# Kernel optimization log

Hardware: AMD Instinct MI355X
Metric: run time of the kernel (lower is better)

The kernel has to match this reference:

```python
import jax, jax.numpy as jnp
import numpy as np

TIMESTEPS = 1000

def _cosine_schedule(T, s=0.008):
    # Nichol & Dhariwal cosine schedule
    x = np.linspace(0.0, T, T + 1, dtype=np.float64)
    acp = np.cos(((x / T) + s) / (1.0 + s) * np.pi / 2.0) ** 2
    acp = acp / acp[0]
    betas = np.clip(1.0 - acp[1:] / acp[:-1], 1e-4, 0.999)
    alphas_cumprod = np.cumprod(1.0 - betas)
    return (betas.astype(np.float32),
            np.sqrt(alphas_cumprod).astype(np.float32),
            np.sqrt(1.0 - alphas_cumprod).astype(np.float32))

BETAS, SQRT_ACP, SQRT_OM_ACP = _cosine_schedule(TIMESTEPS)

B = 2048            # crystals
N_PER = 64          # atoms per crystal (uniform ragged groups)
N = B * N_PER       # total atoms
NODE_DIM = 64
N_SPECIES = 100

def setup_inputs() -> dict:
    key = jax.random.key(0)
    ks = jax.random.split(key, 10)
    frac_coords = jax.random.uniform(ks[0], (N, 3), dtype=jnp.float32)
    noise = jax.random.normal(ks[1], (N, 3), dtype=jnp.float32)
    pred_noise = jax.random.normal(ks[2], (N, 3), dtype=jnp.float32)
    h_final = jax.random.normal(ks[3], (N, NODE_DIM), dtype=jnp.float32)
    # lattice: identity-dominated cells ~5 Angstrom with small perturbation
    lattice = 5.0 * jnp.eye(3, dtype=jnp.float32)[None] + 0.2 * jax.random.normal(ks[4], (B, 3, 3), dtype=jnp.float32)
    W1 = jax.random.normal(ks[5], (NODE_DIM, 128), dtype=jnp.float32) * (1.0 / np.sqrt(NODE_DIM))
    b1 = jnp.zeros((128,), dtype=jnp.float32)
    W2 = jax.random.normal(ks[6], (128, N_SPECIES), dtype=jnp.float32) * (1.0 / np.sqrt(128.0))
    b2 = jnp.zeros((N_SPECIES,), dtype=jnp.float32)
    t = jax.random.randint(ks[7], (B,), 0, TIMESTEPS)
    batch_indices = jnp.repeat(jnp.arange(B), N_PER)
    species = jax.random.randint(ks[8], (N,), 0, N_SPECIES)
    return {"frac_coords": frac_coords, "noise": noise, "pred_noise": pred_noise,
            "h_final": h_final, "lattice": lattice, "W1": W1, "b1": b1,
            "W2": W2, "b2": b2, "t": t, "batch_indices": batch_indices,
            "species": species}

def reference(frac_coords, noise, pred_noise, h_final, lattice, W1, b1, W2, b2,
              t, batch_indices, species):
    sqrt_acp = jnp.asarray(SQRT_ACP)
    sqrt_om = jnp.asarray(SQRT_OM_ACP)
    t_nodes = t[batch_indices]                       # [N]
    sa = sqrt_acp[t_nodes][:, None]                  # [N,1]
    so = sqrt_om[t_nodes][:, None]                   # [N,1]
    # q_sample + periodic wrap
    x_t = sa * frac_coords + so * noise
    x_t = x_t - jnp.floor(x_t)
    # diffusion MSE (dynamics output pred_noise supplied as input)
    loss_diffusion = jnp.mean((pred_noise - noise) ** 2)
    # predicted x0, wrapped
    pred_x0 = (x_t - so * pred_noise) / sa
    pred_x0 = pred_x0 - jnp.floor(pred_x0)
    # vectorized ragged PBC repulsion (uniform groups of N_PER atoms)
    bsz = lattice.shape[0]
    n = frac_coords.shape[0] // bsz
    f = pred_x0.reshape(bsz, n, 3)                   # [B,n,3]
    diff = f[:, :, None, :] - f[:, None, :, :]       # [B,n,n,3]
    diff = diff - jnp.round(diff)                    # minimum-image convention
    diff_c = jnp.einsum('bijk,bkl->bijl', diff, lattice)
    dist_sq = jnp.sum(diff_c ** 2, axis=-1)          # [B,n,n]
    eye = jnp.eye(n, dtype=bool)
    dist_sq = jnp.where(eye[None], 1e10, dist_sq)    # fill_diagonal_(inf)
    dist = jnp.sqrt(dist_sq + 1e-8)
    rep = jax.nn.relu(0.8 - dist) ** 2
    l_repulsion = jnp.sum(rep) / n / bsz
    loss_diffusion = loss_diffusion + 5.0 * l_repulsion
    # species head: Linear -> SiLU -> Linear, cross entropy
    hidden = jax.nn.silu(h_final @ W1 + b1)
    logits = hidden @ W2 + b2                        # [N,100]
    logp = jax.nn.log_softmax(logits, axis=-1)
    loss_species = -jnp.mean(jnp.take_along_axis(logp, species[:, None], axis=-1))
    return (loss_diffusion, loss_species, l_repulsion)
```

## Files before the change

kernel.cpp:

```cpp
#include <hip/hip_runtime.h>
#include <math.h>

#define TSTEPS   1000
#define NB       2048
#define NPER     64
#define NATOMS   (NB*NPER)
#define NDIM     64
#define NHID     128
#define NSPEC    100
#define H_LD     136
#define H_LDS_SHORTS (64*H_LD)

typedef __attribute__((ext_vector_type(8))) short bf16x8;
typedef __attribute__((ext_vector_type(4))) float f32x4;

__device__ inline short f2bf(float x) {
  unsigned u = __builtin_bit_cast(unsigned, x);
  u += 0x7fffu + ((u >> 16) & 1u);
  return (short)(u >> 16);
}

__global__ __launch_bounds__(256) void k_sched(float* __restrict__ sacp,
                                               float* __restrict__ som,
                                               const float* __restrict__ W1,
                                               const float* __restrict__ W2,
                                               unsigned short* __restrict__ w1f,
                                               unsigned short* __restrict__ w2f) {
  const int tid = threadIdx.x, blk = blockIdx.x;
  if (blk == 0) {
    __shared__ double sh[256];
    const double PI = 3.14159265358979323846, s = 0.008;
    const int t0 = tid * 4;
    double lg[4], loc = 0.0;
    if (t0 < TSTEPS) {
      double c[5];
      #pragma unroll
      for (int i = 0; i < 5; ++i) {
        double u = (((double)(t0 + i) / (double)TSTEPS) + s) / (1.0 + s) * PI * 0.5;
        c[i] = cos(u);
      }
      #pragma unroll
      for (int i = 0; i < 4; ++i) {
        double beta = 1.0 - (c[i+1]*c[i+1]) / (c[i]*c[i]);
        beta = fmin(fmax(beta, 1e-4), 0.999);
        lg[i] = log(1.0 - beta);
        loc += lg[i];
      }
    }
    sh[tid] = loc;
    __syncthreads();
    for (int off = 1; off < 256; off <<= 1) {
      double add = (tid >= off) ? sh[tid - off] : 0.0;
      __syncthreads();
      sh[tid] += add;
      __syncthreads();
    }
    if (t0 < TSTEPS) {
      double run = sh[tid] - loc;
      #pragma unroll
      for (int i = 0; i < 4; ++i) {
        run += lg[i];
        double cum = exp(run);
        sacp[t0+i] = (float)sqrt(cum);
        som[t0+i]  = (float)sqrt(1.0 - cum);
      }
    }
  } else if (blk <= 4) {
    const int c0 = (blk - 1) * 256 + tid;
    const int lane = c0 & 63, t = c0 >> 6;
    const int kk = t & 1, nt = t >> 1;
    const int q = lane >> 4, l15 = lane & 15;
    __attribute__((aligned(16))) unsigned short v[8];
    #pragma unroll
    for (int j = 0; j < 8; ++j) {
      int k = kk*32 + q*8 + j;
      v[j] = (unsigned short)f2bf(W1[k*NHID + nt*16 + l15]);
    }
    *(uint4*)(w1f + (size_t)c0*8) = *(const uint4*)v;
  } else {
    for (int c0 = (blk - 5) * 256 + tid; c0 < 3584; c0 += 1792) {
      const int lane = c0 & 63, t = c0 >> 6;
      const int kk = t & 3, nt = t >> 2;
      const int q = lane >> 4, l15 = lane & 15;
      const int cls = nt*16 + l15;
      __attribute__((aligned(16))) unsigned short v[8];
      #pragma unroll
      for (int j = 0; j < 8; ++j) {
        int k = kk*32 + q*8 + j;
        v[j] = (cls < NSPEC) ? (unsigned short)f2bf(W2[k*NSPEC + cls]) : 0;
      }
      *(uint4*)(w2f + (size_t)c0*8) = *(const uint4*)v;
    }
  }
}

__global__ __launch_bounds__(256, 4) void k_main(const float* __restrict__ hfin,
                                                 const float* __restrict__ b1,
                                                 const float* __restrict__ b2,
                                                 const int*   __restrict__ spec,
                                                 const unsigned short* __restrict__ w1f,
                                                 const unsigned short* __restrict__ w2f,
                                                 const float* __restrict__ frac,
                                                 const float* __restrict__ noise,
                                                 const float* __restrict__ pnoise,
                                                 const float* __restrict__ lattice,
                                                 const int*   __restrict__ tarr,
                                                 const float* __restrict__ sacp,
                                                 const float* __restrict__ som,
                                                 float* __restrict__ mseP,
                                                 float* __restrict__ repP,
                                                 float* __restrict__ specP) {
  __shared__ __attribute__((aligned(16))) unsigned short Hs[H_LDS_SHORTS];
  __shared__ float f[NPER*3];
  __shared__ float wred[12];
  const int tid  = threadIdx.x;
  const int wave = tid >> 6, lane = tid & 63;
  const int q = lane >> 4, l15 = lane & 15;
  const int b = blockIdx.x, atomBase = b*64, slabBase = atomBase + wave*16;

  const int tt = tarr[b];
  const float sa = sacp[tt], so = som[tt];
  float msep = 0.0f;
  if (tid < NPER*3) {
    const int gi = b*(NPER*3) + tid;
    float fr = frac[gi], nz = noise[gi], p = pnoise[gi];
    float xt = sa*fr + so*nz;  xt -= floorf(xt);
    float px = (xt - so*p)/sa; px -= floorf(px);
    f[tid] = px;
    float d = p - nz; msep = d*d;
  }

  bf16x8 aF[2];
  {
    const float* rp = hfin + (size_t)(slabBase + l15) * NDIM;
    #pragma unroll
    for (int kk = 0; kk < 2; ++kk) {
      const float4 p = *(const float4*)(rp + kk*32 + q*8);
      const float4 r = *(const float4*)(rp + kk*32 + q*8 + 4);
      bf16x8 a;
      a[0]=f2bf(p.x); a[1]=f2bf(p.y); a[2]=f2bf(p.z); a[3]=f2bf(p.w);
      a[4]=f2bf(r.x); a[5]=f2bf(r.y); a[6]=f2bf(r.z); a[7]=f2bf(r.w);
      aF[kk] = a;
    }
  }

  f32x4 acc1[8];
  #pragma unroll
  for (int nt = 0; nt < 8; ++nt) acc1[nt] = (f32x4){0.f,0.f,0.f,0.f};
  #pragma unroll
  for (int nt = 0; nt < 8; ++nt) {
    #pragma unroll
    for (int kk = 0; kk < 2; ++kk) {
      bf16x8 wa = *(const bf16x8*)(w1f + (size_t)(((nt*2 + kk)*64 + lane))*8);
      acc1[nt] = __builtin_amdgcn_mfma_f32_16x16x32_bf16(wa, aF[kk], acc1[nt], 0, 0, 0);
    }
  }
  #pragma unroll
  for (int nt = 0; nt < 8; ++nt) {
    const float4 bv = *(const float4*)(b1 + nt*16 + q*4);
    float s0, s1, s2, s3;
    { float x = acc1[nt][0] + bv.x; s0 = x / (1.0f + __expf(-x)); }
    { float x = acc1[nt][1] + bv.y; s1 = x / (1.0f + __expf(-x)); }
    { float x = acc1[nt][2] + bv.z; s2 = x / (1.0f + __expf(-x)); }
    { float x = acc1[nt][3] + bv.w; s3 = x / (1.0f + __expf(-x)); }
    uint2 pk;
    pk.x = ((unsigned)(unsigned short)f2bf(s0)) | (((unsigned)(unsigned short)f2bf(s1)) << 16);
    pk.y = ((unsigned)(unsigned short)f2bf(s2)) | (((unsigned)(unsigned short)f2bf(s3)) << 16);
    *(uint2*)(Hs + (wave*16 + l15)*H_LD + nt*16 + q*4) = pk;
  }
  __syncthreads();

  bf16x8 a2[4];
  #pragma unroll
  for (int kk = 0; kk < 4; ++kk)
    a2[kk] = *(const bf16x8*)(Hs + (wave*16 + l15)*H_LD + kk*32 + q*8);
  f32x4 acc2[7];
  #pragma unroll
  for (int nt = 0; nt < 7; ++nt) acc2[nt] = (f32x4){0.f,0.f,0.f,0.f};
  #pragma unroll
  for (int nt = 0; nt < 7; ++nt) {
    #pragma unroll
    for (int kk = 0; kk < 4; ++kk) {
      bf16x8 wb = *(const bf16x8*)(w2f + (size_t)(((nt*4 + kk)*64 + lane))*8);
      acc2[nt] = __builtin_amdgcn_mfma_f32_16x16x32_bf16(wb, a2[kk], acc2[nt], 0, 0, 0);
    }
  }

  const int tgt = spec[slabBase + l15];
  float mx = -1e30f;
  #pragma unroll
  for (int nt = 0; nt < 7; ++nt) {
    float4 bb = {0.f,0.f,0.f,0.f};
    if (nt < 6 || q == 0) bb = *(const float4*)(b2 + nt*16 + q*4);
    #pragma unroll
    for (int r = 0; r < 4; ++r) {
      const int cls = nt*16 + q*4 + r;
      float v = acc2[nt][r] + ((const float*)&bb)[r];
      v = (cls < NSPEC) ? v : -1e30f;
      acc2[nt][r] = v;
      mx = fmaxf(mx, v);
    }
  }
  mx = fmaxf(mx, __shfl_xor(mx, 16, 64));
  mx = fmaxf(mx, __shfl_xor(mx, 32, 64));
  float ssum = 0.0f, lt = 0.0f;
  #pragma unroll
  for (int nt = 0; nt < 7; ++nt) {
    #pragma unroll
    for (int r = 0; r < 4; ++r) {
      float v = acc2[nt][r];
      ssum += __expf(v - mx);
      lt   += (nt*16 + q*4 + r == tgt) ? v : 0.0f;
    }
  }
  ssum += __shfl_xor(ssum, 16, 64);  ssum += __shfl_xor(ssum, 32, 64);
  lt   += __shfl_xor(lt,   16, 64);  lt   += __shfl_xor(lt,   32, 64);
  float logp = lt - mx - __logf(ssum);
  #pragma unroll
  for (int d = 1; d < 16; d <<= 1) logp += __shfl_xor(logp, d, 64);

  const float* L = lattice + b*9;
  const float L00=L[0],L01=L[1],L02=L[2],
              L10=L[3],L11=L[4],L12=L[5],
              L20=L[6],L21=L[7],L22=L[8];
  float rep = 0.0f;
  #pragma unroll 4
  for (int it = 0; it < 16; ++it) {
    const int i = it*4 + wave;
    const int j = lane;
    if (i != j) {
      float dx = f[i*3+0] - f[j*3+0]; dx -= rintf(dx);
      float dy = f[i*3+1] - f[j*3+1]; dy -= rintf(dy);
      float dz = f[i*3+2] - f[j*3+2]; dz -= rintf(dz);
      float cx = dx*L00 + dy*L10 + dz*L20;
      float cy = dx*L01 + dy*L11 + dz*L21;
      float cz = dx*L02 + dy*L12 + dz*L22;
      float dist = sqrtf(cx*cx + cy*cy + cz*cz + 1e-8f);
      float r = 0.8f - dist;
      if (r > 0.0f) rep = fmaf(r, r, rep);
    }
  }
  #pragma unroll
  for (int o = 32; o > 0; o >>= 1) {
    rep  += __shfl_down(rep,  o, 64);
    msep += __shfl_down(msep, o, 64);
  }
  if (lane == 0) { wred[wave] = logp; wred[4+wave] = rep; wred[8+wave] = msep; }
  __syncthreads();
  if (tid == 0) {
    specP[b] = wred[0] + wred[1] + wred[2]  + wred[3];
    repP[b]  = wred[4] + wred[5] + wred[6]  + wred[7];
    mseP[b]  = wred[8] + wred[9] + wred[10] + wred[11];
  }
}

__global__ __launch_bounds__(1024) void k_fin(const float* __restrict__ mseP,
                                              const float* __restrict__ repP,
                                              const float* __restrict__ specP,
                                              float* __restrict__ out) {
  __shared__ double sh[48];
  const int tid = threadIdx.x;
  double m = 0.0, r = 0.0, s = 0.0;
  for (int i = tid; i < NB; i += 1024) {
    m += (double)mseP[i];
    r += (double)repP[i];
    s += (double)specP[i];
  }
  #pragma unroll
  for (int o = 32; o > 0; o >>= 1) {
    m += __shfl_down(m, o, 64);
    r += __shfl_down(r, o, 64);
    s += __shfl_down(s, o, 64);
  }
  const int w = tid >> 6, lane = tid & 63;
  if (lane == 0) { sh[w] = m; sh[16+w] = r; sh[32+w] = s; }
  __syncthreads();
  if (tid == 0) {
    double M=0, R=0, S=0;
    for (int i = 0; i < 16; ++i) { M += sh[i]; R += sh[16+i]; S += sh[32+i]; }
    double mse   = M / (double)(NATOMS*3);
    double lrep  = R / (double)NATOMS;
    double lspec = -S / (double)NATOMS;
    out[0] = (float)(mse + 5.0*lrep);
    out[1] = (float)lspec;
    out[2] = (float)lrep;
  }
}

extern "C" void kernel_launch(void* const* d_in, const int* in_sizes, int n_in,
                              void* d_out, int out_size, void* d_ws, size_t ws_size,
                              hipStream_t stream) {
  const float* frac    = (const float*)d_in[0];
  const float* noise   = (const float*)d_in[1];
  const float* pnoise  = (const float*)d_in[2];
  const float* hfin    = (const float*)d_in[3];
  const float* lattice = (const float*)d_in[4];
  const float* W1      = (const float*)d_in[5];
  const float* b1      = (const float*)d_in[6];
  const float* W2      = (const float*)d_in[7];
  const float* b2      = (const float*)d_in[8];
  const int*   tarr    = (const int*)d_in[9];
  const int*   spec    = (const int*)d_in[11];
  float* out = (float*)d_out;

  float*  sacp = (float*)d_ws;
  float*  som  = sacp + 1024;
  unsigned short* w1f = (unsigned short*)((char*)d_ws + 8192);
  unsigned short* w2f = (unsigned short*)((char*)d_ws + 24576);
  float* mseP  = (float*)((char*)d_ws + 53248);
  float* repP  = (float*)((char*)d_ws + 61440);
  float* specP = (float*)((char*)d_ws + 69632);

  k_sched<<<dim3(12), dim3(256),  0, stream>>>(sacp, som, W1, W2, w1f, w2f);
  k_main <<<dim3(NB), dim3(256),  0, stream>>>(hfin, b1, b2, spec, w1f, w2f,
                                               frac, noise, pnoise, lattice,
                                               tarr, sacp, som, mseP, repP, specP);
  k_fin  <<<dim3(1),  dim3(1024), 0, stream>>>(mseP, repP, specP, out);
}
```

Baseline: 137.1 us.

## Remove block barriers in main kernel using per-wave LDS and shuffles

The block-wide __syncthreads calls are removed. Each wave now keeps its own LDS slice for the hidden activations, laid out to match the MFMA fragments, and uses only a wave barrier. Fractional coordinates stay in registers, one atom per lane, and are broadcast with shuffles for the repulsion loop. Per-wave partial sums go straight to global memory and are reduced in the final kernel. The change also pads b2 in the setup kernel, uses fast reciprocal and sqrt intrinsics, fully unrolls the pair loop, and drops the 4-blocks-per-CU launch bound, so register use may rise and occupancy may change.

```diff
diff --git a/kernel.cpp b/kernel.cpp
--- a/kernel.cpp
+++ b/kernel.cpp
@@ -8,8 +8,6 @@
 #define NDIM     64
 #define NHID     128
 #define NSPEC    100
-#define H_LD     136
-#define H_LDS_SHORTS (64*H_LD)
 
 typedef __attribute__((ext_vector_type(8))) short bf16x8;
 typedef __attribute__((ext_vector_type(4))) float f32x4;
@@ -24,10 +22,13 @@
                                                float* __restrict__ som,
                                                const float* __restrict__ W1,
                                                const float* __restrict__ W2,
+                                               const float* __restrict__ b2,
                                                unsigned short* __restrict__ w1f,
-                                               unsigned short* __restrict__ w2f) {
+                                               unsigned short* __restrict__ w2f,
+                                               float* __restrict__ b2p) {
   const int tid = threadIdx.x, blk = blockIdx.x;
   if (blk == 0) {
+    if (tid < 112) b2p[tid] = (tid < NSPEC) ? b2[tid] : 0.0f;
     __shared__ double sh[256];
     const double PI = 3.14159265358979323846, s = 0.008;
     const int t0 = tid * 4;
@@ -94,40 +95,46 @@
   }
 }
 
-__global__ __launch_bounds__(256, 4) void k_main(const float* __restrict__ hfin,
-                                                 const float* __restrict__ b1,
-                                                 const float* __restrict__ b2,
-                                                 const int*   __restrict__ spec,
-                                                 const unsigned short* __restrict__ w1f,
-                                                 const unsigned short* __restrict__ w2f,
-                                                 const float* __restrict__ frac,
-                                                 const float* __restrict__ noise,
-                                                 const float* __restrict__ pnoise,
-                                                 const float* __restrict__ lattice,
-                                                 const int*   __restrict__ tarr,
-                                                 const float* __restrict__ sacp,
-                                                 const float* __restrict__ som,
-                                                 float* __restrict__ mseP,
-                                                 float* __restrict__ repP,
-                                                 float* __restrict__ specP) {
-  __shared__ __attribute__((aligned(16))) unsigned short Hs[H_LDS_SHORTS];
-  __shared__ float f[NPER*3];
-  __shared__ float wred[12];
+__global__ __launch_bounds__(256) void k_main(const float* __restrict__ hfin,
+                                              const float* __restrict__ b1,
+                                              const float* __restrict__ b2p,
+                                              const int*   __restrict__ spec,
+                                              const unsigned short* __restrict__ w1f,
+                                              const unsigned short* __restrict__ w2f,
+                                              const float* __restrict__ frac,
+                                              const float* __restrict__ noise,
+                                              const float* __restrict__ pnoise,
+                                              const float* __restrict__ lattice,
+                                              const int*   __restrict__ tarr,
+                                              const float* __restrict__ sacp,
+                                              const float* __restrict__ som,
+                                              float* __restrict__ mseP,
+                                              float* __restrict__ repP,
+                                              float* __restrict__ specP) {
+  __shared__ __attribute__((aligned(16))) unsigned short Hs[4*2048];
   const int tid  = threadIdx.x;
   const int wave = tid >> 6, lane = tid & 63;
   const int q = lane >> 4, l15 = lane & 15;
   const int b = blockIdx.x, atomBase = b*64, slabBase = atomBase + wave*16;
+  unsigned short* HsW = Hs + wave*2048;
 
   const int tt = tarr[b];
   const float sa = sacp[tt], so = som[tt];
-  float msep = 0.0f;
-  if (tid < NPER*3) {
-    const int gi = b*(NPER*3) + tid;
-    float fr = frac[gi], nz = noise[gi], p = pnoise[gi];
-    float xt = sa*fr + so*nz;  xt -= floorf(xt);
-    float px = (xt - so*p)/sa; px -= floorf(px);
-    f[tid] = px;
-    float d = p - nz; msep = d*d;
+  const float rsa = __builtin_amdgcn_rcpf(sa);
+  float px0, px1, px2, msep;
+  {
+    const int a = atomBase + lane;
+    const float3 fr = *(const float3*)(frac   + 3*(size_t)a);
+    const float3 nz = *(const float3*)(noise  + 3*(size_t)a);
+    const float3 pn = *(const float3*)(pnoise + 3*(size_t)a);
+    float xt0 = fmaf(so, nz.x, sa*fr.x); xt0 -= floorf(xt0);
+    float xt1 = fmaf(so, nz.y, sa*fr.y); xt1 -= floorf(xt1);
+    float xt2 = fmaf(so, nz.z, sa*fr.z); xt2 -= floorf(xt2);
+    px0 = (xt0 - so*pn.x)*rsa; px0 -= floorf(px0);
+    px1 = (xt1 - so*pn.y)*rsa; px1 -= floorf(px1);
+    px2 = (xt2 - so*pn.z)*rsa; px2 -= floorf(px2);
+    float d0 = pn.x - nz.x, d1 = pn.y - nz.y, d2 = pn.z - nz.z;
+    msep = fmaf(d0, d0, fmaf(d1, d1, d2*d2));
   }
 
   bf16x8 aF[2];
@@ -158,22 +165,24 @@
   #pragma unroll
   for (int nt = 0; nt < 8; ++nt) {
     const float4 bv = *(const float4*)(b1 + nt*16 + q*4);
-    float s0, s1, s2, s3;
-    { float x = acc1[nt][0] + bv.x; s0 = x / (1.0f + __expf(-x)); }
-    { float x = acc1[nt][1] + bv.y; s1 = x / (1.0f + __expf(-x)); }
-    { float x = acc1[nt][2] + bv.z; s2 = x / (1.0f + __expf(-x)); }
-    { float x = acc1[nt][3] + bv.w; s3 = x / (1.0f + __expf(-x)); }
+    float sl[4];
+    #pragma unroll
+    for (int r = 0; r < 4; ++r) {
+      float x = acc1[nt][r] + ((const float*)&bv)[r];
+      float e = __expf(-x);
+      sl[r] = x * __builtin_amdgcn_rcpf(1.0f + e);
+    }
     uint2 pk;
-    pk.x = ((unsigned)(unsigned short)f2bf(s0)) | (((unsigned)(unsigned short)f2bf(s1)) << 16);
-    pk.y = ((unsigned)(unsigned short)f2bf(s2)) | (((unsigned)(unsigned short)f2bf(s3)) << 16);
-    *(uint2*)(Hs + (wave*16 + l15)*H_LD + nt*16 + q*4) = pk;
-  }
-  __syncthreads();
+    pk.x = ((unsigned)(unsigned short)f2bf(sl[0])) | (((unsigned)(unsigned short)f2bf(sl[1])) << 16);
+    pk.y = ((unsigned)(unsigned short)f2bf(sl[2])) | (((unsigned)(unsigned short)f2bf(sl[3])) << 16);
+    *(uint2*)(HsW + (nt*2 + (q>>1))*128 + l15*8 + (q&1)*4) = pk;
+  }
+  __builtin_amdgcn_wave_barrier();
 
   bf16x8 a2[4];
   #pragma unroll
   for (int kk = 0; kk < 4; ++kk)
-    a2[kk] = *(const bf16x8*)(Hs + (wave*16 + l15)*H_LD + kk*32 + q*8);
+    a2[kk] = *(const bf16x8*)(HsW + (kk*4 + q)*128 + l15*8);
   f32x4 acc2[7];
   #pragma unroll
   for (int nt = 0; nt < 7; ++nt) acc2[nt] = (f32x4){0.f,0.f,0.f,0.f};
@@ -190,8 +199,7 @@
   float mx = -1e30f;
   #pragma unroll
   for (int nt = 0; nt < 7; ++nt) {
-    float4 bb = {0.f,0.f,0.f,0.f};
-    if (nt < 6 || q == 0) bb = *(const float4*)(b2 + nt*16 + q*4);
+    const float4 bb = *(const float4*)(b2p + nt*16 + q*4);
     #pragma unroll
     for (int r = 0; r < 4; ++r) {
       const int cls = nt*16 + q*4 + r;
@@ -224,19 +232,21 @@
               L10=L[3],L11=L[4],L12=L[5],
               L20=L[6],L21=L[7],L22=L[8];
   float rep = 0.0f;
-  #pragma unroll 4
+  #pragma unroll
   for (int it = 0; it < 16; ++it) {
-    const int i = it*4 + wave;
-    const int j = lane;
-    if (i != j) {
-      float dx = f[i*3+0] - f[j*3+0]; dx -= rintf(dx);
-      float dy = f[i*3+1] - f[j*3+1]; dy -= rintf(dy);
-      float dz = f[i*3+2] - f[j*3+2]; dz -= rintf(dz);
+    const int i = wave*16 + it;
+    float xi = __shfl(px0, i, 64);
+    float yi = __shfl(px1, i, 64);
+    float zi = __shfl(px2, i, 64);
+    if (i != lane) {
+      float dx = xi - px0; dx -= rintf(dx);
+      float dy = yi - px1; dy -= rintf(dy);
+      float dz = zi - px2; dz -= rintf(dz);
       float cx = dx*L00 + dy*L10 + dz*L20;
       float cy = dx*L01 + dy*L11 + dz*L21;
       float cz = dx*L02 + dy*L12 + dz*L22;
-      float dist = sqrtf(cx*cx + cy*cy + cz*cz + 1e-8f);
-      float r = 0.8f - dist;
+      float d2 = fmaf(cx, cx, fmaf(cy, cy, cz*cz)) + 1e-8f;
+      float r  = 0.8f - __builtin_amdgcn_sqrtf(d2);
       if (r > 0.0f) rep = fmaf(r, r, rep);
     }
   }
@@ -245,12 +255,10 @@
     rep  += __shfl_down(rep,  o, 64);
     msep += __shfl_down(msep, o, 64);
   }
-  if (lane == 0) { wred[wave] = logp; wred[4+wave] = rep; wred[8+wave] = msep; }
-  __syncthreads();
-  if (tid == 0) {
-    specP[b] = wred[0] + wred[1] + wred[2]  + wred[3];
-    repP[b]  = wred[4] + wred[5] + wred[6]  + wred[7];
-    mseP[b]  = wred[8] + wred[9] + wred[10] + wred[11];
+  if (lane == 0) {
+    specP[b*4 + wave] = logp;
+    repP [b*4 + wave] = rep;
+    if (wave == 0) mseP[b] = msep;
   }
 }
 
@@ -261,10 +269,10 @@
   __shared__ double sh[48];
   const int tid = threadIdx.x;
   double m = 0.0, r = 0.0, s = 0.0;
-  for (int i = tid; i < NB; i += 1024) {
-    m += (double)mseP[i];
+  for (int i = tid; i < NB*4; i += 1024) {
     r += (double)repP[i];
     s += (double)specP[i];
+    if (i < NB) m += (double)mseP[i];
   }
   #pragma unroll
   for (int o = 32; o > 0; o >>= 1) {
@@ -307,12 +315,13 @@
   float*  som  = sacp + 1024;
   unsigned short* w1f = (unsigned short*)((char*)d_ws + 8192);
   unsigned short* w2f = (unsigned short*)((char*)d_ws + 24576);
-  float* mseP  = (float*)((char*)d_ws + 53248);
-  float* repP  = (float*)((char*)d_ws + 61440);
-  float* specP = (float*)((char*)d_ws + 69632);
-
-  k_sched<<<dim3(12), dim3(256),  0, stream>>>(sacp, som, W1, W2, w1f, w2f);
-  k_main <<<dim3(NB), dim3(256),  0, stream>>>(hfin, b1, b2, spec, w1f, w2f,
+  float* b2p   = (float*)((char*)d_ws + 53248);
+  float* mseP  = (float*)((char*)d_ws + 53760);
+  float* repP  = (float*)((char*)d_ws + 61952);
+  float* specP = (float*)((char*)d_ws + 94720);
+
+  k_sched<<<dim3(12), dim3(256),  0, stream>>>(sacp, som, W1, W2, b2, w1f, w2f, b2p);
+  k_main <<<dim3(NB), dim3(256),  0, stream>>>(hfin, b1, b2p, spec, w1f, w2f,
                                                frac, noise, pnoise, lattice,
                                                tarr, sacp, som, mseP, repP, specP);
   k_fin  <<<dim3(1),  dim3(1024), 0, stream>>>(mseP, repP, specP, out);
```

After: 128.4 us. 1.07x faster.
